# Optimization experiments

Measured on AMD Instinct MI355X. Metric: run time of the kernel, lower is better.

The kernel has to match this reference:

```python
import jax, jax.numpy as jnp
import numpy as np

MOMENTUM = 0.9
BN_EPS = 1e-5
NORM_EPS = 1e-12
NUM_CLASSES = 10000
DIM_MLP = 512
NUM_EXPERTS = 3
FEAT_DIM = 256
N = 4096


def _l2norm(x, axis=-1):
    # F.normalize: x / max(||x||, eps)
    n = jnp.sqrt(jnp.sum(x * x, axis=axis, keepdims=True))
    return x / jnp.maximum(n, NORM_EPS)


def setup_inputs() -> dict:
    key = jax.random.key(0)
    ks = jax.random.split(key, 8)
    feat_in = jax.random.normal(ks[0], (N, DIM_MLP * NUM_EXPERTS), dtype=jnp.float32)
    label = jax.random.randint(ks[1], (N,), 0, NUM_CLASSES, dtype=jnp.int32)
    # encoder params
    W1 = jax.random.normal(ks[2], (DIM_MLP * NUM_EXPERTS, DIM_MLP), dtype=jnp.float32) / np.sqrt(DIM_MLP * NUM_EXPERTS)
    b1 = jnp.zeros((DIM_MLP,), dtype=jnp.float32)
    gamma = jnp.ones((DIM_MLP,), dtype=jnp.float32)
    beta = jnp.zeros((DIM_MLP,), dtype=jnp.float32)
    W2 = jax.random.normal(ks[3], (DIM_MLP, FEAT_DIM), dtype=jnp.float32) / np.sqrt(DIM_MLP)
    b2 = jnp.zeros((FEAT_DIM,), dtype=jnp.float32)
    # memory bank buffer: randn then row-normalized (as in __init__)
    memory_pt = _l2norm(jax.random.normal(ks[4], (NUM_CLASSES, FEAT_DIM), dtype=jnp.float32))
    return {"feat_in": feat_in, "label": label, "W1": W1, "b1": b1,
            "gamma": gamma, "beta": beta, "W2": W2, "b2": b2,
            "memory_pt": memory_pt}


def _encoder(feat_in, W1, b1, gamma, beta, W2, b2):
    h = feat_in @ W1 + b1                       # [N, dim_mlp]
    # BatchNorm1d in training mode: batch statistics (biased variance)
    mu = jnp.mean(h, axis=0)
    var = jnp.mean((h - mu) ** 2, axis=0)
    h = (h - mu) * jax.lax.rsqrt(var + BN_EPS) * gamma + beta
    h = jax.nn.relu(h)
    out = h @ W2 + b2                           # [N, 256]
    return _l2norm(out, axis=1)


def _update_memory(memory_pt, feat, label):
    # Strictly sequential per-sample momentum update (order matters for
    # duplicate labels), each touched row renormalized — lax.scan recurrence.
    def step(mem, xy):
        x, y = xy
        pt = MOMENTUM * mem[y] + (1.0 - MOMENTUM) * x
        pt = _l2norm(pt, axis=0)
        return mem.at[y].set(pt), None
    mem, _ = jax.lax.scan(step, memory_pt, (feat, label))
    return mem


def reference(feat_in, label, W1, b1, gamma, beta, W2, b2, memory_pt):
    feat = _encoder(feat_in, W1, b1, gamma, beta, W2, b2)   # [N, 256], unit rows
    # memory_pt.detach(): no grad flows through the memory bank
    mem = _update_memory(jax.lax.stop_gradient(memory_pt),
                         jax.lax.stop_gradient(feat), label)
    mem = jax.lax.stop_gradient(mem)
    sim_logit = jnp.einsum('nc,kc->nk', feat, mem)          # [N, K]
    return sim_logit
```

## Files before the change

### kernel.cpp

```cpp
#include <hip/hip_runtime.h>
#include <stdint.h>

typedef _Float16 f16;
typedef _Float16 f16x4 __attribute__((ext_vector_type(4)));
typedef _Float16 f16x8 __attribute__((ext_vector_type(8)));
typedef float f32x4 __attribute__((ext_vector_type(4)));

typedef __attribute__((address_space(1))) void gvoid;
typedef __attribute__((address_space(3))) void lvoid;

#define NROWS 4096
#define DIMIN 1536
#define DMLP 512
#define FDIM 256
#define NCLS 10000
#define NPAD 10112
#define NBMW 320

__device__ __forceinline__ void load_lds16(const void* g, void* l) {
    __builtin_amdgcn_global_load_lds((gvoid*)g, (lvoid*)l, 16, 0, 0);
}

template<int TM, int TN, bool STATS, bool NT, bool SWAP>
__global__ __launch_bounds__(256) void gemm_t(
    const f16* __restrict__ A, const f16* __restrict__ Bt,
    float* __restrict__ C, const float* __restrict__ bias,
    int K, int ldc, int Nstore,
    float* __restrict__ sums, float* __restrict__ sqs)
{
    constexpr int BK = 64;
    constexpr int AM = TM / 32;
    constexpr int AN = TN / 32;
    constexpr int CA = TM * 8;
    constexpr int CB = TN * 8;
    constexpr int RTOT = (CA + CB) / 256;
    constexpr int SPAN = (TM + TN) * BK;
    static_assert(CA % 256 == 0, "A/B staging split must be round-aligned");
    static_assert(!(SWAP && STATS), "SWAP epilogue has no STATS path");

    __shared__ f16 smem[2 * SPAN];

    const int tid  = threadIdx.x;
    const int lane = tid & 63;
    const int w    = tid >> 6;
    const int wm   = (w >> 1) * (TM / 2);
    const int wn   = (w & 1) * (TN / 2);
    const int row0 = blockIdx.x * TM;
    const int col0 = blockIdx.y * TN;
    const int quad = lane >> 4;
    const int r16  = lane & 15;

    f32x4 acc[AM][AN] = {};

    const f16* gsrc[RTOT];
    int ldsoff[RTOT];
#pragma unroll
    for (int r = 0; r < RTOT; ++r) {
        int c = tid + r * 256;
        bool isA = (c < CA);
        int cc = isA ? c : c - CA;
        int row = cc >> 3;
        int gs = (cc & 7) ^ (row & 7);
        gsrc[r] = (isA ? A + (size_t)(row0 + row) * K
                       : Bt + (size_t)(col0 + row) * K) + gs * 8;
        ldsoff[r] = (isA ? 0 : TM * BK) + cc * 8;
    }

    const int nt = K / BK;

#pragma unroll
    for (int r = 0; r < RTOT; ++r)
        load_lds16(gsrc[r], smem + ldsoff[r]);
    __syncthreads();

    int buf = 0;
    for (int t = 0; t < nt; ++t) {
        if (t + 1 < nt) {
            const int k0 = (t + 1) * BK;
            const int o = (buf ^ 1) * SPAN;
#pragma unroll
            for (int r = 0; r < RTOT; ++r)
                load_lds16(gsrc[r] + k0, smem + o + ldsoff[r]);
        }
        const f16* As = smem + buf * SPAN;
        const f16* Bs = As + TM * BK;
#pragma unroll
        for (int ks = 0; ks < 2; ++ks) {
            f16x8 af[AM], bq[AN];
#pragma unroll
            for (int mi = 0; mi < AM; ++mi) {
                int row = wm + mi * 16 + r16;
                int slot = (ks * 4 + quad) ^ (r16 & 7);
                af[mi] = *(const f16x8*)&As[row * BK + slot * 8];
            }
#pragma unroll
            for (int ni = 0; ni < AN; ++ni) {
                int row = wn + ni * 16 + r16;
                int slot = (ks * 4 + quad) ^ (r16 & 7);
                bq[ni] = *(const f16x8*)&Bs[row * BK + slot * 8];
            }
#pragma unroll
            for (int mi = 0; mi < AM; ++mi)
#pragma unroll
                for (int ni = 0; ni < AN; ++ni) {
                    if constexpr (SWAP)
                        acc[mi][ni] = __builtin_amdgcn_mfma_f32_16x16x32_f16(
                            bq[ni], af[mi], acc[mi][ni], 0, 0, 0);
                    else
                        acc[mi][ni] = __builtin_amdgcn_mfma_f32_16x16x32_f16(
                            af[mi], bq[ni], acc[mi][ni], 0, 0, 0);
                }
        }
        __syncthreads();
        buf ^= 1;
    }

    if constexpr (SWAP) {
#pragma unroll
        for (int ni = 0; ni < AN; ++ni) {
            int c0 = col0 + wn + ni * 16 + quad * 4;
            if (c0 < Nstore) {
#pragma unroll
                for (int mi = 0; mi < AM; ++mi) {
                    int m = row0 + wm + mi * 16 + r16;
                    if constexpr (NT)
                        __builtin_nontemporal_store(acc[mi][ni],
                            (f32x4*)&C[(size_t)m * ldc + c0]);
                    else
                        *(f32x4*)&C[(size_t)m * ldc + c0] = acc[mi][ni];
                }
            }
        }
    } else {
#pragma unroll
        for (int ni = 0; ni < AN; ++ni) {
            int col = col0 + wn + ni * 16 + r16;
            float bv = bias ? bias[col] : 0.0f;
            float s = 0.0f, q = 0.0f;
            if (col < Nstore) {
#pragma unroll
                for (int mi = 0; mi < AM; ++mi) {
                    int rowb = row0 + wm + mi * 16 + quad * 4;
#pragma unroll
                    for (int r = 0; r < 4; ++r) {
                        float v = acc[mi][ni][r] + bv;
                        if constexpr (NT)
                            __builtin_nontemporal_store(v, &C[(size_t)(rowb + r) * ldc + col]);
                        else
                            C[(size_t)(rowb + r) * ldc + col] = v;
                        if constexpr (STATS) { s += v; q += v * v; }
                    }
                }
            }
            if constexpr (STATS) {
                s += __shfl_xor(s, 16); s += __shfl_xor(s, 32);
                q += __shfl_xor(q, 16); q += __shfl_xor(q, 32);
                if (quad == 0) {
                    atomicAdd(&sums[col], s);
                    atomicAdd(&sqs[col], q);
                }
            }
        }
    }
}

__device__ __forceinline__ void transpose_tile(
    const float* __restrict__ in, f16* __restrict__ out,
    int R, int C, int bxx, int byy, float* t, int tid)
{
    int tx = tid & 31, ty = tid >> 5;
    int c0 = bxx * 32, r0 = byy * 32;
#pragma unroll
    for (int k = 0; k < 4; ++k)
        t[(ty + k * 8) * 33 + tx] = in[(size_t)(r0 + ty + k * 8) * C + c0 + tx];
    __syncthreads();
#pragma unroll
    for (int k = 0; k < 4; ++k)
        out[(size_t)(c0 + ty + k * 8) * R + r0 + tx] = (f16)t[tx * 33 + ty + k * 8];
}

__global__ void setup_k(const float* __restrict__ feat_in, f16* __restrict__ A1h,
                        const float* __restrict__ W1, f16* __restrict__ W1t,
                        const float* __restrict__ W2, f16* __restrict__ W2t,
                        const int* __restrict__ label, float* __restrict__ stats,
                        unsigned int* __restrict__ bm)
{
    __shared__ float t[32 * 33];
    const int b = blockIdx.x, tid = threadIdx.x;
    if (b < 6144) {
        int i = b * 256 + tid;
        float4 v = *(const float4*)&feat_in[(size_t)i * 4];
        f16x4 o = {(f16)v.x, (f16)v.y, (f16)v.z, (f16)v.w};
        *(f16x4*)&A1h[(size_t)i * 4] = o;
    } else if (b < 6912) {
        int idx = b - 6144;
        transpose_tile(W1, W1t, DIMIN, DMLP, idx & 15, idx >> 4, t, tid);
    } else if (b < 7040) {
        int idx = b - 6912;
        transpose_tile(W2, W2t, DMLP, FDIM, idx & 7, idx >> 3, t, tid);
    } else {
        unsigned int* lbm = (unsigned int*)t;
        for (int i = tid; i < NBMW; i += 256) lbm[i] = 0u;
        for (int i = tid; i < 2 * DMLP; i += 256) stats[i] = 0.0f;
        __syncthreads();
        for (int i = tid; i < NROWS; i += 256) {
            int y = label[i];
            atomicOr(&lbm[y >> 5], 1u << (y & 31));
        }
        __syncthreads();
        for (int i = tid; i < NBMW; i += 256) bm[i] = lbm[i];
    }
}

__global__ void bn_apply_k(const float* __restrict__ h,
                           const float* __restrict__ sums, const float* __restrict__ sqs,
                           const float* __restrict__ gamma, const float* __restrict__ beta,
                           f16* __restrict__ out) {
    int i = blockIdx.x * 256 + threadIdx.x;
    int c = (i & 127) * 4;
    const float inv_n = 1.0f / 4096.0f;
    float4 s4 = *(const float4*)&sums[c];
    float4 q4 = *(const float4*)&sqs[c];
    float4 g4 = *(const float4*)&gamma[c];
    float4 b4 = *(const float4*)&beta[c];
    float4 sc, sh;
    {
        float mu = s4.x * inv_n, var = fmaxf(q4.x * inv_n - mu * mu, 0.0f);
        float a = rsqrtf(var + 1e-5f) * g4.x; sc.x = a; sh.x = b4.x - mu * a;
    }
    {
        float mu = s4.y * inv_n, var = fmaxf(q4.y * inv_n - mu * mu, 0.0f);
        float a = rsqrtf(var + 1e-5f) * g4.y; sc.y = a; sh.y = b4.y - mu * a;
    }
    {
        float mu = s4.z * inv_n, var = fmaxf(q4.z * inv_n - mu * mu, 0.0f);
        float a = rsqrtf(var + 1e-5f) * g4.z; sc.z = a; sh.z = b4.z - mu * a;
    }
    {
        float mu = s4.w * inv_n, var = fmaxf(q4.w * inv_n - mu * mu, 0.0f);
        float a = rsqrtf(var + 1e-5f) * g4.w; sc.w = a; sh.w = b4.w - mu * a;
    }
    float4 v = *(const float4*)&h[(size_t)i * 4];
    f16x4 o = {(f16)fmaxf(v.x * sc.x + sh.x, 0.0f),
               (f16)fmaxf(v.y * sc.y + sh.y, 0.0f),
               (f16)fmaxf(v.z * sc.z + sh.z, 0.0f),
               (f16)fmaxf(v.w * sc.w + sh.w, 0.0f)};
    *(f16x4*)&out[(size_t)i * 4] = o;
}

__global__ void l2norm_k(const float* __restrict__ X, float* __restrict__ Y, f16* __restrict__ Yh) {
    int wv = (blockIdx.x * 256 + threadIdx.x) >> 6;
    int lane = threadIdx.x & 63;
    float4 v = *(const float4*)&X[(size_t)wv * FDIM + lane * 4];
    float s = v.x * v.x + v.y * v.y + v.z * v.z + v.w * v.w;
#pragma unroll
    for (int off = 32; off > 0; off >>= 1) s += __shfl_xor(s, off);
    float inv = 1.0f / fmaxf(sqrtf(s), 1e-12f);
    float4 o = {v.x * inv, v.y * inv, v.z * inv, v.w * inv};
    *(float4*)&Y[(size_t)wv * FDIM + lane * 4] = o;
    f16x4 oh = {(f16)o.x, (f16)o.y, (f16)o.z, (f16)o.w};
    *(f16x4*)&Yh[(size_t)wv * FDIM + lane * 4] = oh;
}

__global__ void chain_k(const int* __restrict__ label, const float* __restrict__ feat,
                        const float* __restrict__ mp, const unsigned int* __restrict__ bm,
                        f16* __restrict__ memh) {
    int y = (blockIdx.x * 256 + threadIdx.x) >> 6;
    int lane = threadIdx.x & 63;
    float4 m = {0.f, 0.f, 0.f, 0.f};
    if (y < NCLS) {
        m = *(const float4*)&mp[(size_t)y * FDIM + lane * 4];
        if ((bm[y >> 5] >> (y & 31)) & 1u) {
            for (int g = 0; g < 64; ++g) {
                int lab = label[g * 64 + lane];
                unsigned long long mask = __ballot(lab == y);
                while (mask) {
                    int b = __builtin_ctzll(mask);
                    mask &= mask - 1;
                    int i = g * 64 + b;
                    float4 x = *(const float4*)&feat[(size_t)i * FDIM + lane * 4];
                    m.x = 0.9f * m.x + 0.1f * x.x;
                    m.y = 0.9f * m.y + 0.1f * x.y;
                    m.z = 0.9f * m.z + 0.1f * x.z;
                    m.w = 0.9f * m.w + 0.1f * x.w;
                    float s = m.x * m.x + m.y * m.y + m.z * m.z + m.w * m.w;
#pragma unroll
                    for (int off = 32; off > 0; off >>= 1) s += __shfl_xor(s, off);
                    float inv = 1.0f / fmaxf(sqrtf(s), 1e-12f);
                    m.x *= inv; m.y *= inv; m.z *= inv; m.w *= inv;
                }
            }
        }
    }
    f16x4 o = {(f16)m.x, (f16)m.y, (f16)m.z, (f16)m.w};
    *(f16x4*)&memh[(size_t)y * FDIM + lane * 4] = o;
}

extern "C" void kernel_launch(void* const* d_in, const int* in_sizes, int n_in,
                              void* d_out, int out_size, void* d_ws, size_t ws_size,
                              hipStream_t stream) {
    const float* feat_in = (const float*)d_in[0];
    const int*   label   = (const int*)d_in[1];
    const float* W1      = (const float*)d_in[2];
    const float* b1      = (const float*)d_in[3];
    const float* gamma   = (const float*)d_in[4];
    const float* beta    = (const float*)d_in[5];
    const float* W2      = (const float*)d_in[6];
    const float* b2      = (const float*)d_in[7];
    const float* mp      = (const float*)d_in[8];
    float* out = (float*)d_out;

    char* w = (char*)d_ws;
    f16* A1h   = (f16*)w;   w += (size_t)NROWS * DIMIN * 2;
    f16* W1t   = (f16*)w;   w += (size_t)DMLP * DIMIN * 2;
    f16* W2t   = (f16*)w;   w += (size_t)FDIM * DMLP * 2;
    float* h   = (float*)w; w += (size_t)NROWS * DMLP * 4;
    f16* h2    = (f16*)w;   w += (size_t)NROWS * DMLP * 2;
    float* out2= (float*)w; w += (size_t)NROWS * FDIM * 4;
    float* feat= (float*)w; w += (size_t)NROWS * FDIM * 4;
    f16* feath = (f16*)w;   w += (size_t)NROWS * FDIM * 2;
    f16* memh  = (f16*)w;   w += (size_t)NPAD * FDIM * 2;
    float* sums= (float*)w; w += DMLP * 4;
    float* sqs = (float*)w; w += DMLP * 4;
    unsigned int* bm = (unsigned int*)w; w += NBMW * 4;

    setup_k<<<7041, 256, 0, stream>>>(feat_in, A1h, W1, W1t, W2, W2t,
                                      label, sums, bm);

    {
        dim3 g(NROWS / 128, DMLP / 64);
        gemm_t<128, 64, true, false, false><<<g, 256, 0, stream>>>(
            A1h, W1t, h, b1, DIMIN, DMLP, DMLP, sums, sqs);
    }

    bn_apply_k<<<(NROWS * DMLP / 4) / 256, 256, 0, stream>>>(
        h, sums, sqs, gamma, beta, h2);

    {
        dim3 g(NROWS / 64, FDIM / 64);
        gemm_t<64, 64, false, false, false><<<g, 256, 0, stream>>>(
            h2, W2t, out2, b2, DMLP, FDIM, FDIM, nullptr, nullptr);
    }

    l2norm_k<<<NROWS / 4, 256, 0, stream>>>(out2, feat, feath);

    chain_k<<<NPAD / 4, 256, 0, stream>>>(label, feat, mp, bm, memh);

    {
        dim3 g(NROWS / 128, NPAD / 128);
        gemm_t<128, 128, false, true, true><<<g, 256, 0, stream>>>(
            feath, memh, out, nullptr, FDIM, NCLS, NCLS, nullptr, nullptr);
    }
}
```

Before: 293.3 us.

## Add XCD-aware tile swizzle to GEMMs and drop fp32 feat buffer

Each GEMM now runs on a 1D grid, and each block's linear id is remapped so that every XCD gets a contiguous chunk of tiles. The A-major or B-major order is chosen per GEMM, with the aim of raising L2 reuse of the shared operand tiles on each die. Separately, the l2norm kernel no longer writes an fp32 copy of the features, and the memory-bank chain update reads the fp16 features instead. This removes one fp32 write and shrinks the chain reads, but the momentum update now uses reduced-precision inputs.

```diff
diff --git a/kernel.cpp b/kernel.cpp
--- a/kernel.cpp
+++ b/kernel.cpp
@@ -21,7 +21,7 @@
     __builtin_amdgcn_global_load_lds((gvoid*)g, (lvoid*)l, 16, 0, 0);
 }
 
-template<int TM, int TN, bool STATS, bool NT, bool SWAP>
+template<int TM, int TN, int NBX, int NBY, bool STATS, bool NT, bool SWAP, bool AMAJ>
 __global__ __launch_bounds__(256) void gemm_t(
     const f16* __restrict__ A, const f16* __restrict__ Bt,
     float* __restrict__ C, const float* __restrict__ bias,
@@ -35,7 +35,10 @@
     constexpr int CB = TN * 8;
     constexpr int RTOT = (CA + CB) / 256;
     constexpr int SPAN = (TM + TN) * BK;
+    constexpr int NTILES = NBX * NBY;
+    constexpr int CHUNK = NTILES / 8;
     static_assert(CA % 256 == 0, "A/B staging split must be round-aligned");
+    static_assert(NTILES % 8 == 0, "bijective XCD swizzle needs %8==0");
     static_assert(!(SWAP && STATS), "SWAP epilogue has no STATS path");
 
     __shared__ f16 smem[2 * SPAN];
@@ -45,8 +48,13 @@
     const int w    = tid >> 6;
     const int wm   = (w >> 1) * (TM / 2);
     const int wn   = (w & 1) * (TN / 2);
-    const int row0 = blockIdx.x * TM;
-    const int col0 = blockIdx.y * TN;
+    const int lin  = blockIdx.x;
+    const int tile = (lin & 7) * CHUNK + (lin >> 3);
+    int bx, by;
+    if constexpr (AMAJ) { bx = tile / NBY; by = tile % NBY; }
+    else               { by = tile / NBX; bx = tile % NBX; }
+    const int row0 = bx * TM;
+    const int col0 = by * TN;
     const int quad = lane >> 4;
     const int r16  = lane & 15;
 
@@ -248,7 +256,7 @@
     *(f16x4*)&out[(size_t)i * 4] = o;
 }
 
-__global__ void l2norm_k(const float* __restrict__ X, float* __restrict__ Y, f16* __restrict__ Yh) {
+__global__ void l2norm_k(const float* __restrict__ X, f16* __restrict__ Yh) {
     int wv = (blockIdx.x * 256 + threadIdx.x) >> 6;
     int lane = threadIdx.x & 63;
     float4 v = *(const float4*)&X[(size_t)wv * FDIM + lane * 4];
@@ -256,13 +264,12 @@
 #pragma unroll
     for (int off = 32; off > 0; off >>= 1) s += __shfl_xor(s, off);
     float inv = 1.0f / fmaxf(sqrtf(s), 1e-12f);
-    float4 o = {v.x * inv, v.y * inv, v.z * inv, v.w * inv};
-    *(float4*)&Y[(size_t)wv * FDIM + lane * 4] = o;
-    f16x4 oh = {(f16)o.x, (f16)o.y, (f16)o.z, (f16)o.w};
+    f16x4 oh = {(f16)(v.x * inv), (f16)(v.y * inv),
+                (f16)(v.z * inv), (f16)(v.w * inv)};
     *(f16x4*)&Yh[(size_t)wv * FDIM + lane * 4] = oh;
 }
 
-__global__ void chain_k(const int* __restrict__ label, const float* __restrict__ feat,
+__global__ void chain_k(const int* __restrict__ label, const f16* __restrict__ feath,
                         const float* __restrict__ mp, const unsigned int* __restrict__ bm,
                         f16* __restrict__ memh) {
     int y = (blockIdx.x * 256 + threadIdx.x) >> 6;
@@ -278,11 +285,11 @@
                     int b = __builtin_ctzll(mask);
                     mask &= mask - 1;
                     int i = g * 64 + b;
-                    float4 x = *(const float4*)&feat[(size_t)i * FDIM + lane * 4];
-                    m.x = 0.9f * m.x + 0.1f * x.x;
-                    m.y = 0.9f * m.y + 0.1f * x.y;
-                    m.z = 0.9f * m.z + 0.1f * x.z;
-                    m.w = 0.9f * m.w + 0.1f * x.w;
+                    f16x4 xr = *(const f16x4*)&feath[(size_t)i * FDIM + lane * 4];
+                    m.x = 0.9f * m.x + 0.1f * (float)xr[0];
+                    m.y = 0.9f * m.y + 0.1f * (float)xr[1];
+                    m.z = 0.9f * m.z + 0.1f * (float)xr[2];
+                    m.w = 0.9f * m.w + 0.1f * (float)xr[3];
                     float s = m.x * m.x + m.y * m.y + m.z * m.z + m.w * m.w;
 #pragma unroll
                     for (int off = 32; off > 0; off >>= 1) s += __shfl_xor(s, off);
@@ -317,7 +324,6 @@
     float* h   = (float*)w; w += (size_t)NROWS * DMLP * 4;
     f16* h2    = (f16*)w;   w += (size_t)NROWS * DMLP * 2;
     float* out2= (float*)w; w += (size_t)NROWS * FDIM * 4;
-    float* feat= (float*)w; w += (size_t)NROWS * FDIM * 4;
     f16* feath = (f16*)w;   w += (size_t)NROWS * FDIM * 2;
     f16* memh  = (f16*)w;   w += (size_t)NPAD * FDIM * 2;
     float* sums= (float*)w; w += DMLP * 4;
@@ -327,28 +333,19 @@
     setup_k<<<7041, 256, 0, stream>>>(feat_in, A1h, W1, W1t, W2, W2t,
                                       label, sums, bm);
 
-    {
-        dim3 g(NROWS / 128, DMLP / 64);
-        gemm_t<128, 64, true, false, false><<<g, 256, 0, stream>>>(
-            A1h, W1t, h, b1, DIMIN, DMLP, DMLP, sums, sqs);
-    }
+    gemm_t<128, 64, 32, 8, true, false, false, true><<<256, 256, 0, stream>>>(
+        A1h, W1t, h, b1, DIMIN, DMLP, DMLP, sums, sqs);
 
     bn_apply_k<<<(NROWS * DMLP / 4) / 256, 256, 0, stream>>>(
         h, sums, sqs, gamma, beta, h2);
 
-    {
-        dim3 g(NROWS / 64, FDIM / 64);
-        gemm_t<64, 64, false, false, false><<<g, 256, 0, stream>>>(
-            h2, W2t, out2, b2, DMLP, FDIM, FDIM, nullptr, nullptr);
-    }
-
-    l2norm_k<<<NROWS / 4, 256, 0, stream>>>(out2, feat, feath);
-
-    chain_k<<<NPAD / 4, 256, 0, stream>>>(label, feat, mp, bm, memh);
-
-    {
-        dim3 g(NROWS / 128, NPAD / 128);
-        gemm_t<128, 128, false, true, true><<<g, 256, 0, stream>>>(
-            feath, memh, out, nullptr, FDIM, NCLS, NCLS, nullptr, nullptr);
-    }
-}
+    gemm_t<64, 64, 64, 4, false, false, false, true><<<256, 256, 0, stream>>>(
+        h2, W2t, out2, b2, DMLP, FDIM, FDIM, nullptr, nullptr);
+
+    l2norm_k<<<NROWS / 4, 256, 0, stream>>>(out2, feath);
+
+    chain_k<<<NPAD / 4, 256, 0, stream>>>(label, feath, mp, bm, memh);
+
+    gemm_t<128, 128, 32, 79, false, true, true, false><<<2528, 256, 0, stream>>>(
+        feath, memh, out, nullptr, FDIM, NCLS, NCLS, nullptr, nullptr);
+}
```

Result: no change. 291.9 us (-0.5%).
